# Optimization experiments

Measured on AMD Instinct MI355X. Metric: run time of the kernel, lower is better.

Reference implementation:

```python
import jax, jax.numpy as jnp
import numpy as np

L, B, D = 1024, 32, 1024
USE_TANH = True  # use_tanh=1

def setup_inputs() -> dict:
    key = jax.random.key(0)
    k1, k2, k3, k4 = jax.random.split(key, 4)
    return {
        "x": jax.random.normal(k1, (L, B, D), jnp.float32),
        "c0": jax.random.normal(k2, (B, D), jnp.float32),
        "weight": jax.random.normal(k3, (D, D, 3), jnp.float32) * 0.02,
        "bias": jax.random.normal(k4, (2 * D,), jnp.float32) * 0.02,
    }

def reference(x, c0, weight, bias):
    # x: [L,B,D], weight: [D_in, D_out, 3], bias: [2*D_out], c0: [B,D_out]
    d = weight.shape[1]
    # u = x @ weight.view(n_in, 3*n_out) with per-output-dim interleaving -> [L,B,D,3]
    u = jnp.einsum('lbi,iok->lbok', x, weight)
    u0 = u[..., 0]                       # candidate
    f = jax.nn.sigmoid(u[..., 1] + bias[:d])    # forget gate
    r = jax.nn.sigmoid(u[..., 2] + bias[d:])    # highway/reset gate

    def step(c_prev, inp):
        f_t, u0_t = inp
        c_t = f_t * c_prev + (1.0 - f_t) * u0_t
        return c_t, c_t

    _, c = jax.lax.scan(step, c0, (f, u0))  # c: [L,B,D]
    g = jnp.tanh(c) if USE_TANH else c
    h = r * g + (1.0 - r) * x               # highway connection (n_in == n_out path)
    return h, c
```

## Files before the change

kernel.cpp:

```cpp
#include <hip/hip_runtime.h>
#include <hip/hip_bf16.h>
#include <stdint.h>

#define L_DIM 1024
#define B_DIM 32
#define D_DIM 1024
#define M_DIM (L_DIM * B_DIM)
#define N3_DIM (3 * D_DIM)
#define K_DIM D_DIM
#define LBD ((int64_t)L_DIM * B_DIM * D_DIM)
#define NBD (B_DIM * D_DIM)
#define NCHUNK 32
#define CLEN 32

#define BM 256
#define BN 256
#define BK 64
#define NMT (M_DIM / BM)
#define NNT (N3_DIM / BN)
#define NKT (K_DIM / BK)

typedef __bf16 bf16_t;
typedef bf16_t bf16x8 __attribute__((ext_vector_type(8)));
typedef float f32x4 __attribute__((ext_vector_type(4)));

__device__ __forceinline__ unsigned short f2bf(float f) {
    union { float f; unsigned u; } v; v.f = f;
    unsigned u = v.u;
    u += 0x7FFFu + ((u >> 16) & 1u);
    return (unsigned short)(u >> 16);
}
__device__ __forceinline__ float bf2f(unsigned short h) {
    union { unsigned u; float f; } v; v.u = ((unsigned)h) << 16;
    return v.f;
}

__global__ void cvt_x_kernel(const float* __restrict__ x, unsigned short* __restrict__ xb) {
    int64_t i0 = ((int64_t)blockIdx.x * blockDim.x + threadIdx.x) * 4;
    int64_t stride = (int64_t)gridDim.x * blockDim.x * 4;
    for (int64_t i = i0; i < LBD; i += stride) {
        float4 v = *reinterpret_cast<const float4*>(x + i);
        ushort4 o;
        o.x = f2bf(v.x); o.y = f2bf(v.y); o.z = f2bf(v.z); o.w = f2bf(v.w);
        *reinterpret_cast<ushort4*>(xb + i) = o;
    }
}

__global__ void cvt_w_kernel(const float* __restrict__ w, unsigned short* __restrict__ wT) {
    __shared__ float tile[64][65];
    int bid = blockIdx.x;
    int k  = bid >> 8;
    int o0 = ((bid >> 4) & 15) * 64;
    int i0 = (bid & 15) * 64;
    int t = threadIdx.x;
    {
        int o = t & 63, ib = t >> 6;
        #pragma unroll
        for (int it = 0; it < 16; ++it) {
            int i = ib + it * 4;
            tile[o][i] = w[((int64_t)(i0 + i) * 1024 + (o0 + o)) * 3 + k];
        }
    }
    __syncthreads();
    {
        int i = t & 63, ob = t >> 6;
        #pragma unroll
        for (int ot = 0; ot < 16; ++ot) {
            int o = ob + ot * 4;
            wT[(int64_t)(k * 1024 + o0 + o) * 1024 + (i0 + i)] = f2bf(tile[o][i]);
        }
    }
}

__device__ __forceinline__ void gload_lds16(const void* g, void* l) {
    __builtin_amdgcn_global_load_lds(
        (const __attribute__((address_space(1))) unsigned int*)g,
        (__attribute__((address_space(3))) unsigned int*)l,
        16, 0, 0);
}

__global__ __launch_bounds__(512, 2) void gemm_kernel(
    const unsigned short* __restrict__ A,
    const unsigned short* __restrict__ Bt,
    const float* __restrict__ bias,
    float* __restrict__ u0_out,
    unsigned short* __restrict__ fb,
    unsigned short* __restrict__ rb)
{
    __shared__ unsigned short a_lds[2][BM * BK];
    __shared__ unsigned short b_lds[2][BM * BK];

    int bid = blockIdx.x;
    int swz = (bid & 7) * (NMT * NNT / 8) + (bid >> 3);
    int nt = swz % NNT, mt = swz / NNT;
    int m0 = mt * BM, n0 = nt * BN;

    int tid = threadIdx.x;
    int w = tid >> 6, lane = tid & 63;
    int wm = w >> 2, wn = w & 3;
    int l15 = lane & 15, l4 = lane >> 4;

    int sr = lane >> 3;
    int scol = ((lane & 7) ^ sr) << 3;
    const unsigned short* Abase = A  + (int64_t)(m0 + w * 32 + sr) * K_DIM + scol;
    const unsigned short* Bbase = Bt + (int64_t)(n0 + w * 32 + sr) * K_DIM + scol;

    f32x4 acc[8][4];
    #pragma unroll
    for (int i = 0; i < 8; ++i)
        #pragma unroll
        for (int j = 0; j < 4; ++j) acc[i][j] = (f32x4){0.f, 0.f, 0.f, 0.f};

    #pragma unroll
    for (int i = 0; i < 4; ++i) {
        gload_lds16(Abase + (int64_t)i * 8 * K_DIM,      &a_lds[0][(w * 32 + i * 8) * BK]);
        gload_lds16(Bbase + (int64_t)i * 8 * K_DIM,      &b_lds[0][(w * 32 + i * 8) * BK]);
    }
    #pragma unroll
    for (int i = 0; i < 4; ++i) {
        gload_lds16(Abase + (int64_t)i * 8 * K_DIM + BK, &a_lds[1][(w * 32 + i * 8) * BK]);
        gload_lds16(Bbase + (int64_t)i * 8 * K_DIM + BK, &b_lds[1][(w * 32 + i * 8) * BK]);
    }

    #pragma unroll
    for (int kt = 0; kt < NKT; ++kt) {
        int cur = kt & 1;
        if (kt < NKT - 1) asm volatile("s_waitcnt vmcnt(8)" ::: "memory");
        else              asm volatile("s_waitcnt vmcnt(0)" ::: "memory");
        __builtin_amdgcn_s_barrier();
        asm volatile("" ::: "memory");

        const unsigned short* al = a_lds[cur];
        const unsigned short* bl = b_lds[cur];
        __builtin_amdgcn_s_setprio(1);
        #pragma unroll
        for (int ks = 0; ks < 2; ++ks) {
            int pc = (((ks * 4 + l4) ^ (l15 & 7)) << 3);
            bf16x8 bfr[4];
            #pragma unroll
            for (int j = 0; j < 4; ++j)
                bfr[j] = *reinterpret_cast<const bf16x8*>(&bl[(wn * 64 + j * 16 + l15) * BK + pc]);
            #pragma unroll
            for (int i = 0; i < 8; ++i) {
                bf16x8 afr = *reinterpret_cast<const bf16x8*>(&al[(wm * 128 + i * 16 + l15) * BK + pc]);
                #pragma unroll
                for (int j = 0; j < 4; ++j)
                    acc[i][j] = __builtin_amdgcn_mfma_f32_16x16x32_bf16(afr, bfr[j], acc[i][j], 0, 0, 0);
            }
        }
        __builtin_amdgcn_s_setprio(0);
        asm volatile("" ::: "memory");
        __builtin_amdgcn_s_barrier();

        if (kt + 2 < NKT) {
            int64_t k0 = (int64_t)(kt + 2) * BK;
            #pragma unroll
            for (int i = 0; i < 4; ++i) {
                gload_lds16(Abase + (int64_t)i * 8 * K_DIM + k0, &a_lds[cur][(w * 32 + i * 8) * BK]);
                gload_lds16(Bbase + (int64_t)i * 8 * K_DIM + k0, &b_lds[cur][(w * 32 + i * 8) * BK]);
            }
        }
    }

    int region = n0 >> 10;
    #pragma unroll
    for (int i = 0; i < 8; ++i) {
        #pragma unroll
        for (int j = 0; j < 4; ++j) {
            f32x4 v = acc[i][j];
            int row0 = m0 + wm * 128 + i * 16 + l4 * 4;
            int col  = (n0 + wn * 64 + j * 16 + l15) & 1023;
            #pragma unroll
            for (int jj = 0; jj < 4; ++jj) {
                int64_t idx = (int64_t)(row0 + jj) * 1024 + col;
                float val = v[jj];
                if (region == 0) {
                    u0_out[idx] = val;
                } else if (region == 1) {
                    fb[idx] = f2bf(1.0f / (1.0f + __expf(-(val + bias[col]))));
                } else {
                    rb[idx] = f2bf(1.0f / (1.0f + __expf(-(val + bias[1024 + col]))));
                }
            }
        }
    }
}


__global__ void scan_phase1(const unsigned short* __restrict__ fb,
                            const float* __restrict__ u0_arr,
                            float* __restrict__ Aout, float* __restrict__ Bout) {
    int t = blockIdx.x * blockDim.x + threadIdx.x;
    int idx = t & (NBD - 1);
    int chunk = t >> 15;
    int64_t base = (int64_t)chunk * CLEN * NBD + idx;
    float Ap = 1.0f, Bv = 0.0f;
    #pragma unroll 8
    for (int i = 0; i < CLEN; ++i, base += NBD) {
        float f = bf2f(fb[base]);
        float u0 = u0_arr[base];
        Bv = u0 + f * (Bv - u0);
        Ap *= f;
    }
    Aout[t] = Ap; Bout[t] = Bv;
}

__global__ void scan_phase2(const float* __restrict__ c0, const float* __restrict__ Aarr,
                            const float* __restrict__ Barr, float* __restrict__ cin) {
    int idx = blockIdx.x * blockDim.x + threadIdx.x;
    float c = c0[idx];
    #pragma unroll
    for (int ch = 0; ch < NCHUNK; ++ch) {
        cin[ch * NBD + idx] = c;
        c = Aarr[ch * NBD + idx] * c + Barr[ch * NBD + idx];
    }
}

__global__ void scan_phase3(const float* __restrict__ x,
                            const unsigned short* __restrict__ fb,
                            const unsigned short* __restrict__ rb,
                            const float* __restrict__ cin,
                            float* __restrict__ out_h, float* __restrict__ out_c) {
    int t = blockIdx.x * blockDim.x + threadIdx.x;
    int idx = t & (NBD - 1);
    int chunk = t >> 15;
    float c = cin[t];
    int64_t base = (int64_t)chunk * CLEN * NBD + idx;
    #pragma unroll 4
    for (int i = 0; i < CLEN; ++i, base += NBD) {
        float f  = bf2f(fb[base]);
        float u0 = out_c[base];
        c = u0 + f * (c - u0);
        out_c[base] = c;
        float e = __expf(2.0f * c);
        float g = (e - 1.0f) / (e + 1.0f);
        float r = bf2f(rb[base]);
        float xv = x[base];
        out_h[base] = xv + r * (g - xv);
    }
}

extern "C" void kernel_launch(void* const* d_in, const int* in_sizes, int n_in,
                              void* d_out, int out_size, void* d_ws, size_t ws_size,
                              hipStream_t stream) {
    const float* x    = (const float*)d_in[0];
    const float* c0   = (const float*)d_in[1];
    const float* wgt  = (const float*)d_in[2];
    const float* bias = (const float*)d_in[3];
    float* out = (float*)d_out;

    unsigned short* xb = (unsigned short*)d_ws;
    unsigned short* wT = xb + (int64_t)M_DIM * K_DIM;
    unsigned short* fb = wT + (int64_t)N3_DIM * K_DIM;
    unsigned short* rb = fb + LBD;

    float* Aarr = (float*)d_ws;
    float* Barr = Aarr + NCHUNK * NBD;
    float* cin  = Barr + NCHUNK * NBD;

    cvt_x_kernel<<<8192, 256, 0, stream>>>(x, xb);
    cvt_w_kernel<<<768, 256, 0, stream>>>(wgt, wT);
    gemm_kernel<<<NMT * NNT, 512, 0, stream>>>(xb, wT, bias, out + LBD, fb, rb);
    scan_phase1<<<(NCHUNK * NBD) / 256, 256, 0, stream>>>(fb, out + LBD, Aarr, Barr);
    scan_phase2<<<NBD / 256, 256, 0, stream>>>(c0, Aarr, Barr, cin);
    scan_phase3<<<(NCHUNK * NBD) / 256, 256, 0, stream>>>(x, fb, rb, cin, out, out + LBD);
}
```

Before: 560.1 us.

## Restructure GEMM mainloop into half-tile quadrant schedule with fine-grained LDS staging

The GEMM main loop is rebuilt in the style of an 8-wave ping-pong schedule. Each 256x256 tile is split into two 128-row halves of A and of B, and the k-loop runs as four MFMA quadrants per k-step. Loads for the next half-tiles are issued between quadrants, with explicit lgkmcnt/vmcnt waits and barriers, so global-to-LDS traffic and LDS reads overlap with MFMA work. Warp ownership of output rows and columns changes to match, and the epilogue indexing is updated. This adds many more barriers and tight wait-count dependencies, which could stall waves if the counts are off.

```diff
diff --git a/kernel.cpp b/kernel.cpp
--- a/kernel.cpp
+++ b/kernel.cpp
@@ -19,6 +19,7 @@
 #define NMT (M_DIM / BM)
 #define NNT (N3_DIM / BN)
 #define NKT (K_DIM / BK)
+#define NITER (NKT / 2)
 
 typedef __bf16 bf16_t;
 typedef bf16_t bf16x8 __attribute__((ext_vector_type(8)));
@@ -79,6 +80,11 @@
         16, 0, 0);
 }
 
+#define BARRIER() do { asm volatile("" ::: "memory"); __builtin_amdgcn_s_barrier(); asm volatile("" ::: "memory"); } while (0)
+#define WAIT_LGKM0() asm volatile("s_waitcnt lgkmcnt(0)" ::: "memory")
+#define WAIT_LGKM8() asm volatile("s_waitcnt lgkmcnt(8)" ::: "memory")
+#define VMCNT(n) asm volatile("s_waitcnt vmcnt(" #n ")" ::: "memory")
+
 __global__ __launch_bounds__(512, 2) void gemm_kernel(
     const unsigned short* __restrict__ A,
     const unsigned short* __restrict__ Bt,
@@ -87,8 +93,8 @@
     unsigned short* __restrict__ fb,
     unsigned short* __restrict__ rb)
 {
-    __shared__ unsigned short a_lds[2][BM * BK];
-    __shared__ unsigned short b_lds[2][BM * BK];
+    __shared__ __align__(16) unsigned short a_lds[2][2][128 * 64];
+    __shared__ __align__(16) unsigned short b_lds[2][2][128 * 64];
 
     int bid = blockIdx.x;
     int swz = (bid & 7) * (NMT * NNT / 8) + (bid >> 3);
@@ -99,11 +105,40 @@
     int w = tid >> 6, lane = tid & 63;
     int wm = w >> 2, wn = w & 3;
     int l15 = lane & 15, l4 = lane >> 4;
-
-    int sr = lane >> 3;
-    int scol = ((lane & 7) ^ sr) << 3;
-    const unsigned short* Abase = A  + (int64_t)(m0 + w * 32 + sr) * K_DIM + scol;
-    const unsigned short* Bbase = Bt + (int64_t)(n0 + w * 32 + sr) * K_DIM + scol;
+    int pcx = l15 & 7;
+
+    int srow = w * 8 + (lane >> 3);
+    int scol = ((lane & 7) ^ ((lane >> 3) & 7)) << 3;
+    const unsigned short* Asrc = A  + (int64_t)(m0 + srow) * K_DIM + scol;
+    const unsigned short* Bsrc = Bt + (int64_t)(n0 + srow) * K_DIM + scol;
+    unsigned short* dstA = &a_lds[0][0][0] + w * 8 * 64;
+    unsigned short* dstB = &b_lds[0][0][0] + w * 8 * 64;
+
+    auto stageA = [&](int buf, int half, int kt) {
+        if (kt >= NKT) return;
+        const unsigned short* s = Asrc + (int64_t)half * 128 * K_DIM + kt * BK;
+        unsigned short* d = dstA + (buf * 2 + half) * (128 * 64);
+        gload_lds16(s, d);
+        gload_lds16(s + (int64_t)64 * K_DIM, d + 64 * 64);
+    };
+    auto stageB = [&](int buf, int half, int kt) {
+        if (kt >= NKT) return;
+        const unsigned short* s = Bsrc + (int64_t)half * 128 * K_DIM + kt * BK;
+        unsigned short* d = dstB + (buf * 2 + half) * (128 * 64);
+        gload_lds16(s, d);
+        gload_lds16(s + (int64_t)64 * K_DIM, d + 64 * 64);
+    };
+
+    auto rdA_ = [&](int buf, int mh, int im, int ks) -> bf16x8 {
+        int rr = wm * 64 + im * 16 + l15;
+        int pc = ((ks * 4 + l4) ^ pcx) << 3;
+        return *reinterpret_cast<const bf16x8*>(&a_lds[buf][mh][rr * 64 + pc]);
+    };
+    auto rdB_ = [&](int buf, int nh, int jn, int ks) -> bf16x8 {
+        int rr = wn * 32 + jn * 16 + l15;
+        int pc = ((ks * 4 + l4) ^ pcx) << 3;
+        return *reinterpret_cast<const bf16x8*>(&b_lds[buf][nh][rr * 64 + pc]);
+    };
 
     f32x4 acc[8][4];
     #pragma unroll
@@ -111,65 +146,106 @@
         #pragma unroll
         for (int j = 0; j < 4; ++j) acc[i][j] = (f32x4){0.f, 0.f, 0.f, 0.f};
 
-    #pragma unroll
-    for (int i = 0; i < 4; ++i) {
-        gload_lds16(Abase + (int64_t)i * 8 * K_DIM,      &a_lds[0][(w * 32 + i * 8) * BK]);
-        gload_lds16(Bbase + (int64_t)i * 8 * K_DIM,      &b_lds[0][(w * 32 + i * 8) * BK]);
-    }
-    #pragma unroll
-    for (int i = 0; i < 4; ++i) {
-        gload_lds16(Abase + (int64_t)i * 8 * K_DIM + BK, &a_lds[1][(w * 32 + i * 8) * BK]);
-        gload_lds16(Bbase + (int64_t)i * 8 * K_DIM + BK, &b_lds[1][(w * 32 + i * 8) * BK]);
-    }
-
-    #pragma unroll
-    for (int kt = 0; kt < NKT; ++kt) {
-        int cur = kt & 1;
-        if (kt < NKT - 1) asm volatile("s_waitcnt vmcnt(8)" ::: "memory");
-        else              asm volatile("s_waitcnt vmcnt(0)" ::: "memory");
-        __builtin_amdgcn_s_barrier();
-        asm volatile("" ::: "memory");
-
-        const unsigned short* al = a_lds[cur];
-        const unsigned short* bl = b_lds[cur];
-        __builtin_amdgcn_s_setprio(1);
-        #pragma unroll
-        for (int ks = 0; ks < 2; ++ks) {
-            int pc = (((ks * 4 + l4) ^ (l15 & 7)) << 3);
-            bf16x8 bfr[4];
-            #pragma unroll
-            for (int j = 0; j < 4; ++j)
-                bfr[j] = *reinterpret_cast<const bf16x8*>(&bl[(wn * 64 + j * 16 + l15) * BK + pc]);
-            #pragma unroll
-            for (int i = 0; i < 8; ++i) {
-                bf16x8 afr = *reinterpret_cast<const bf16x8*>(&al[(wm * 128 + i * 16 + l15) * BK + pc]);
-                #pragma unroll
-                for (int j = 0; j < 4; ++j)
-                    acc[i][j] = __builtin_amdgcn_mfma_f32_16x16x32_bf16(afr, bfr[j], acc[i][j], 0, 0, 0);
-            }
-        }
-        __builtin_amdgcn_s_setprio(0);
-        asm volatile("" ::: "memory");
-        __builtin_amdgcn_s_barrier();
-
-        if (kt + 2 < NKT) {
-            int64_t k0 = (int64_t)(kt + 2) * BK;
-            #pragma unroll
-            for (int i = 0; i < 4; ++i) {
-                gload_lds16(Abase + (int64_t)i * 8 * K_DIM + k0, &a_lds[cur][(w * 32 + i * 8) * BK]);
-                gload_lds16(Bbase + (int64_t)i * 8 * K_DIM + k0, &b_lds[cur][(w * 32 + i * 8) * BK]);
-            }
-        }
+    bf16x8 af[4][2], b0[2][2], b1[2][2];
+
+#define QUAD(MH, NH, BB)                                                            \
+    do {                                                                            \
+        __builtin_amdgcn_s_setprio(1);                                              \
+        _Pragma("unroll")                                                           \
+        for (int im = 0; im < 4; ++im)                                              \
+            _Pragma("unroll")                                                       \
+            for (int jn = 0; jn < 2; ++jn)                                          \
+                _Pragma("unroll")                                                   \
+                for (int ks = 0; ks < 2; ++ks)                                      \
+                    acc[(MH)*4 + im][(NH)*2 + jn] =                                 \
+                        __builtin_amdgcn_mfma_f32_16x16x32_bf16(                    \
+                            af[im][ks], BB[jn][ks], acc[(MH)*4 + im][(NH)*2 + jn],  \
+                            0, 0, 0);                                               \
+        __builtin_amdgcn_s_setprio(0);                                              \
+    } while (0)
+
+    stageA(0, 0, 0);
+    stageB(0, 0, 0);
+    stageB(0, 1, 0);
+    stageA(0, 1, 0);
+    stageA(1, 0, 1);
+    stageB(1, 0, 1);
+    stageB(1, 1, 1);
+    VMCNT(6);
+    BARRIER();
+
+    for (int t = 0; t < NITER; ++t) {
+        int t2 = t * 2;
+        #pragma unroll
+        for (int im = 0; im < 4; ++im) { af[im][0] = rdA_(0, 0, im, 0); af[im][1] = rdA_(0, 0, im, 1); }
+        #pragma unroll
+        for (int jn = 0; jn < 2; ++jn) { b0[jn][0] = rdB_(0, 0, jn, 0); b0[jn][1] = rdB_(0, 0, jn, 1); }
+        stageA(1, 1, t2 + 1);
+        WAIT_LGKM8();
+        BARRIER();
+        WAIT_LGKM0();
+        QUAD(0, 0, b0);
+        BARRIER();
+        #pragma unroll
+        for (int jn = 0; jn < 2; ++jn) { b1[jn][0] = rdB_(0, 1, jn, 0); b1[jn][1] = rdB_(0, 1, jn, 1); }
+        stageA(0, 0, t2 + 2);
+        BARRIER();
+        WAIT_LGKM0();
+        QUAD(0, 1, b1);
+        BARRIER();
+        #pragma unroll
+        for (int im = 0; im < 4; ++im) { af[im][0] = rdA_(0, 1, im, 0); af[im][1] = rdA_(0, 1, im, 1); }
+        stageB(0, 0, t2 + 2);
+        BARRIER();
+        WAIT_LGKM0();
+        QUAD(1, 0, b0);
+        BARRIER();
+        stageB(0, 1, t2 + 2);
+        if (t < NITER - 1) { VMCNT(6); } else { VMCNT(0); }
+        BARRIER();
+        QUAD(1, 1, b1);
+        BARRIER();
+        #pragma unroll
+        for (int im = 0; im < 4; ++im) { af[im][0] = rdA_(1, 0, im, 0); af[im][1] = rdA_(1, 0, im, 1); }
+        #pragma unroll
+        for (int jn = 0; jn < 2; ++jn) { b0[jn][0] = rdB_(1, 0, jn, 0); b0[jn][1] = rdB_(1, 0, jn, 1); }
+        stageA(0, 1, t2 + 2);
+        WAIT_LGKM8();
+        BARRIER();
+        WAIT_LGKM0();
+        QUAD(0, 0, b0);
+        BARRIER();
+        #pragma unroll
+        for (int jn = 0; jn < 2; ++jn) { b1[jn][0] = rdB_(1, 1, jn, 0); b1[jn][1] = rdB_(1, 1, jn, 1); }
+        stageA(1, 0, t2 + 3);
+        BARRIER();
+        WAIT_LGKM0();
+        QUAD(0, 1, b1);
+        BARRIER();
+        #pragma unroll
+        for (int im = 0; im < 4; ++im) { af[im][0] = rdA_(1, 1, im, 0); af[im][1] = rdA_(1, 1, im, 1); }
+        stageB(1, 0, t2 + 3);
+        BARRIER();
+        WAIT_LGKM0();
+        QUAD(1, 0, b0);
+        BARRIER();
+        stageB(1, 1, t2 + 3);
+        if (t < NITER - 1) { VMCNT(6); } else { VMCNT(0); }
+        BARRIER();
+        QUAD(1, 1, b1);
+        BARRIER();
     }
 
     int region = n0 >> 10;
     #pragma unroll
     for (int i = 0; i < 8; ++i) {
+        int mh = i >> 2, im = i & 3;
         #pragma unroll
         for (int j = 0; j < 4; ++j) {
+            int nh = j >> 1, jn = j & 1;
             f32x4 v = acc[i][j];
-            int row0 = m0 + wm * 128 + i * 16 + l4 * 4;
-            int col  = (n0 + wn * 64 + j * 16 + l15) & 1023;
+            int row0 = m0 + mh * 128 + wm * 64 + im * 16 + l4 * 4;
+            int col  = (n0 + nh * 128 + wn * 32 + jn * 16 + l15) & 1023;
             #pragma unroll
             for (int jj = 0; jj < 4; ++jj) {
                 int64_t idx = (int64_t)(row0 + jj) * 1024 + col;
@@ -184,6 +260,7 @@
             }
         }
     }
+#undef QUAD
 }
 
 
```

Result: faster. 518.0 us (-7.5%).

## Shrink GEMM tile to 128x128 single-buffered with XCD-aware tile mapping

Applied to the files above, without the earlier changes.

Replaces the 256x256 double-buffered GEMM tile (512 threads, async prefetch two stages ahead) with a 128x128 single-buffered tile using 256 threads and synchronous load-then-compute per K step. Block-to-tile mapping is changed so each XCD handles three adjacent N tiles across M rows. This cuts LDS and register use per block and raises block count, but removes the load/compute overlap and lowers arithmetic intensity per tile.

```diff
diff --git a/kernel.cpp b/kernel.cpp
--- a/kernel.cpp
+++ b/kernel.cpp
@@ -13,8 +13,8 @@
 #define NCHUNK 32
 #define CLEN 32
 
-#define BM 256
-#define BN 256
+#define BM 128
+#define BN 128
 #define BK 64
 #define NMT (M_DIM / BM)
 #define NNT (N3_DIM / BN)
@@ -79,7 +79,7 @@
         16, 0, 0);
 }
 
-__global__ __launch_bounds__(512, 2) void gemm_kernel(
+__global__ __launch_bounds__(256, 2) void gemm_kernel(
     const unsigned short* __restrict__ A,
     const unsigned short* __restrict__ Bt,
     const float* __restrict__ bias,
@@ -87,89 +87,70 @@
     unsigned short* __restrict__ fb,
     unsigned short* __restrict__ rb)
 {
-    __shared__ unsigned short a_lds[2][BM * BK];
-    __shared__ unsigned short b_lds[2][BM * BK];
+    __shared__ __align__(16) unsigned short a_tile[128 * 64];
+    __shared__ __align__(16) unsigned short b_tile[128 * 64];
 
     int bid = blockIdx.x;
-    int swz = (bid & 7) * (NMT * NNT / 8) + (bid >> 3);
-    int nt = swz % NNT, mt = swz / NNT;
+    int xcd = bid & 7, local = bid >> 3;
+    int nt = xcd * 3 + (local % 3);
+    int mt = local / 3;
     int m0 = mt * BM, n0 = nt * BN;
 
     int tid = threadIdx.x;
     int w = tid >> 6, lane = tid & 63;
-    int wm = w >> 2, wn = w & 3;
+    int wr = (w >> 1) * 64, wc = (w & 1) * 64;
     int l15 = lane & 15, l4 = lane >> 4;
+    int pcx = l15 & 7;
 
     int sr = lane >> 3;
-    int scol = ((lane & 7) ^ sr) << 3;
-    const unsigned short* Abase = A  + (int64_t)(m0 + w * 32 + sr) * K_DIM + scol;
-    const unsigned short* Bbase = Bt + (int64_t)(n0 + w * 32 + sr) * K_DIM + scol;
-
-    f32x4 acc[8][4];
+    int sc = ((lane & 7) ^ sr) << 3;
+    const unsigned short* Abase = A  + (int64_t)(m0 + sr) * K_DIM + sc;
+    const unsigned short* Bbase = Bt + (int64_t)(n0 + sr) * K_DIM + sc;
+
+    f32x4 acc[4][4];
     #pragma unroll
-    for (int i = 0; i < 8; ++i)
+    for (int i = 0; i < 4; ++i)
         #pragma unroll
         for (int j = 0; j < 4; ++j) acc[i][j] = (f32x4){0.f, 0.f, 0.f, 0.f};
 
-    #pragma unroll
-    for (int i = 0; i < 4; ++i) {
-        gload_lds16(Abase + (int64_t)i * 8 * K_DIM,      &a_lds[0][(w * 32 + i * 8) * BK]);
-        gload_lds16(Bbase + (int64_t)i * 8 * K_DIM,      &b_lds[0][(w * 32 + i * 8) * BK]);
-    }
-    #pragma unroll
-    for (int i = 0; i < 4; ++i) {
-        gload_lds16(Abase + (int64_t)i * 8 * K_DIM + BK, &a_lds[1][(w * 32 + i * 8) * BK]);
-        gload_lds16(Bbase + (int64_t)i * 8 * K_DIM + BK, &b_lds[1][(w * 32 + i * 8) * BK]);
-    }
-
-    #pragma unroll
     for (int kt = 0; kt < NKT; ++kt) {
-        int cur = kt & 1;
-        if (kt < NKT - 1) asm volatile("s_waitcnt vmcnt(8)" ::: "memory");
-        else              asm volatile("s_waitcnt vmcnt(0)" ::: "memory");
-        __builtin_amdgcn_s_barrier();
-        asm volatile("" ::: "memory");
-
-        const unsigned short* al = a_lds[cur];
-        const unsigned short* bl = b_lds[cur];
-        __builtin_amdgcn_s_setprio(1);
+        int k0 = kt * BK;
+        __syncthreads();
+        #pragma unroll
+        for (int i = 0; i < 4; ++i) {
+            int r0 = (i * 4 + w) * 8;
+            gload_lds16(Abase + (int64_t)r0 * K_DIM + k0, &a_tile[r0 * 64]);
+            gload_lds16(Bbase + (int64_t)r0 * K_DIM + k0, &b_tile[r0 * 64]);
+        }
+        __syncthreads();
+
         #pragma unroll
         for (int ks = 0; ks < 2; ++ks) {
-            int pc = (((ks * 4 + l4) ^ (l15 & 7)) << 3);
-            bf16x8 bfr[4];
-            #pragma unroll
-            for (int j = 0; j < 4; ++j)
-                bfr[j] = *reinterpret_cast<const bf16x8*>(&bl[(wn * 64 + j * 16 + l15) * BK + pc]);
-            #pragma unroll
-            for (int i = 0; i < 8; ++i) {
-                bf16x8 afr = *reinterpret_cast<const bf16x8*>(&al[(wm * 128 + i * 16 + l15) * BK + pc]);
+            int pc = ((ks * 4 + l4) ^ pcx) << 3;
+            bf16x8 af[4], bf[4];
+            #pragma unroll
+            for (int im = 0; im < 4; ++im)
+                af[im] = *reinterpret_cast<const bf16x8*>(&a_tile[(wr + im * 16 + l15) * 64 + pc]);
+            #pragma unroll
+            for (int jn = 0; jn < 4; ++jn)
+                bf[jn] = *reinterpret_cast<const bf16x8*>(&b_tile[(wc + jn * 16 + l15) * 64 + pc]);
+            #pragma unroll
+            for (int im = 0; im < 4; ++im)
                 #pragma unroll
-                for (int j = 0; j < 4; ++j)
-                    acc[i][j] = __builtin_amdgcn_mfma_f32_16x16x32_bf16(afr, bfr[j], acc[i][j], 0, 0, 0);
-            }
-        }
-        __builtin_amdgcn_s_setprio(0);
-        asm volatile("" ::: "memory");
-        __builtin_amdgcn_s_barrier();
-
-        if (kt + 2 < NKT) {
-            int64_t k0 = (int64_t)(kt + 2) * BK;
-            #pragma unroll
-            for (int i = 0; i < 4; ++i) {
-                gload_lds16(Abase + (int64_t)i * 8 * K_DIM + k0, &a_lds[cur][(w * 32 + i * 8) * BK]);
-                gload_lds16(Bbase + (int64_t)i * 8 * K_DIM + k0, &b_lds[cur][(w * 32 + i * 8) * BK]);
-            }
+                for (int jn = 0; jn < 4; ++jn)
+                    acc[im][jn] = __builtin_amdgcn_mfma_f32_16x16x32_bf16(
+                        af[im], bf[jn], acc[im][jn], 0, 0, 0);
         }
     }
 
     int region = n0 >> 10;
     #pragma unroll
-    for (int i = 0; i < 8; ++i) {
-        #pragma unroll
-        for (int j = 0; j < 4; ++j) {
-            f32x4 v = acc[i][j];
-            int row0 = m0 + wm * 128 + i * 16 + l4 * 4;
-            int col  = (n0 + wn * 64 + j * 16 + l15) & 1023;
+    for (int im = 0; im < 4; ++im) {
+        #pragma unroll
+        for (int jn = 0; jn < 4; ++jn) {
+            f32x4 v = acc[im][jn];
+            int row0 = m0 + wr + im * 16 + l4 * 4;
+            int col  = (n0 + wc + jn * 16 + l15) & 1023;
             #pragma unroll
             for (int jj = 0; jj < 4; ++jj) {
                 int64_t idx = (int64_t)(row0 + jj) * 1024 + col;
@@ -260,7 +241,7 @@
 
     cvt_x_kernel<<<8192, 256, 0, stream>>>(x, xb);
     cvt_w_kernel<<<768, 256, 0, stream>>>(wgt, wT);
-    gemm_kernel<<<NMT * NNT, 512, 0, stream>>>(xb, wT, bias, out + LBD, fb, rb);
+    gemm_kernel<<<NMT * NNT, 256, 0, stream>>>(xb, wT, bias, out + LBD, fb, rb);
     scan_phase1<<<(NCHUNK * NBD) / 256, 256, 0, stream>>>(fb, out + LBD, Aarr, Barr);
     scan_phase2<<<NBD / 256, 256, 0, stream>>>(c0, Aarr, Barr, cin);
     scan_phase3<<<(NCHUNK * NBD) / 256, 256, 0, stream>>>(x, fb, rb, cin, out, out + LBD);
```

Result: faster. 506.0 us (-9.6%).
